# Kernel optimization log

Measured on AMD Instinct MI355X. Metric: run time of the kernel, lower is better.

The kernel has to match this reference:

```python
import jax, jax.numpy as jnp
import numpy as np
from jax import lax

B, T, D, H, K = 8, 1024, 1024, 16, 3
DK = D // H


def setup_inputs() -> dict:
    key = jax.random.key(0)
    ks = jax.random.split(key, 12)
    s = 0.02
    queries = jax.random.normal(ks[0], (B, T, D), dtype=jnp.float32)
    keys = jax.random.normal(ks[1], (B, T, D), dtype=jnp.float32)
    values = jax.random.normal(ks[2], (B, T, D), dtype=jnp.float32)
    # causal mask: True = masked (strict upper triangle)
    attn_mask = jnp.triu(jnp.ones((T, T), dtype=bool), k=1)
    # key padding mask: last 128 keys padded for every batch element
    src_key_padding_mask = jnp.broadcast_to(jnp.arange(T) >= T - 128, (B, T))
    conv_q_w = jax.random.normal(ks[3], (D, D, K), dtype=jnp.float32) * s  # (out, in, k)
    conv_q_b = jax.random.normal(ks[4], (D,), dtype=jnp.float32) * s
    conv_k_w = jax.random.normal(ks[5], (D, D, K), dtype=jnp.float32) * s
    conv_k_b = jax.random.normal(ks[6], (D,), dtype=jnp.float32) * s
    v_w = jax.random.normal(ks[7], (D, D), dtype=jnp.float32) * s   # torch Linear weight [out,in]
    v_b = jax.random.normal(ks[8], (D,), dtype=jnp.float32) * s
    out_w = jax.random.normal(ks[9], (D, D), dtype=jnp.float32) * s
    out_b = jax.random.normal(ks[10], (D,), dtype=jnp.float32) * s
    return {"queries": queries, "keys": keys, "values": values,
            "attn_mask": attn_mask, "src_key_padding_mask": src_key_padding_mask,
            "conv_q_w": conv_q_w, "conv_q_b": conv_q_b,
            "conv_k_w": conv_k_w, "conv_k_b": conv_k_b,
            "v_w": v_w, "v_b": v_b, "out_w": out_w, "out_b": out_b}


def _conv1d_same(x, w, b):
    # x: [B, T, D] -> conv over time with 'same' padding (pad_l=(K-1)//2, pad_r=K//2)
    pad_l, pad_r = (K - 1) // 2, K // 2
    xc = jnp.pad(x.transpose(0, 2, 1), ((0, 0), (0, 0), (pad_l, pad_r)))  # [B, D, T+K-1]
    y = lax.conv_general_dilated(xc, w, window_strides=(1,), padding='VALID',
                                 dimension_numbers=('NCH', 'OIH', 'NCH'))  # [B, D, T]
    return y.transpose(0, 2, 1) + b  # [B, T, D]


def _attention(queries, keys, values, attn_mask, key_padding_mask,
               conv_q_w, conv_q_b, conv_k_w, conv_k_b, v_w, v_b, out_w, out_b):
    q_out = _conv1d_same(queries, conv_q_w, conv_q_b)  # [B, Tq, D]
    k_out = _conv1d_same(keys, conv_k_w, conv_k_b)     # [B, Tk, D]
    v_out = values @ v_w.T + v_b                        # [B, Tk, D]

    Q = q_out.reshape(B, T, H, DK).transpose(0, 2, 1, 3)  # [B, H, Tq, dk]
    Kh = k_out.reshape(B, T, H, DK).transpose(0, 2, 1, 3)
    V = v_out.reshape(B, T, H, DK).transpose(0, 2, 1, 3)

    scores = jnp.einsum('bhqd,bhkd->bhqk', Q, Kh) / jnp.sqrt(jnp.float32(DK))
    neg = jnp.float32(-jnp.inf)
    scores = jnp.where(key_padding_mask[:, None, None, :], neg, scores)
    scores = jnp.where(attn_mask[None, None, :, :], neg, scores)
    attn_weights = jax.nn.softmax(scores, axis=-1)  # dropout is identity at eval
    attn_output = jnp.einsum('bhqk,bhkd->bhqd', attn_weights, V)
    attn_output = attn_output.transpose(0, 2, 1, 3).reshape(B, T, D)
    return attn_output @ out_w.T + out_b, attn_weights


def reference(queries, keys, values, attn_mask, src_key_padding_mask,
              conv_q_w, conv_q_b, conv_k_w, conv_k_b, v_w, v_b, out_w, out_b):
    return _attention(queries, keys, values, attn_mask, src_key_padding_mask,
                      conv_q_w, conv_q_b, conv_k_w, conv_k_b, v_w, v_b, out_w, out_b)
```

## Files before the change

### kernel.cpp

```cpp
#include <hip/hip_runtime.h>

typedef unsigned short u16;
typedef unsigned int   u32;
typedef __bf16 bf16x8 __attribute__((ext_vector_type(8)));
typedef float  f32x4  __attribute__((ext_vector_type(4)));
typedef const __attribute__((address_space(1))) u32* gas1_t;
typedef __attribute__((address_space(3))) u32*       las3_t;

#define DEV static __device__ __forceinline__
#define MFMA16(a, b, c) __builtin_amdgcn_mfma_f32_16x16x32_bf16((a), (b), (c), 0, 0, 0)

DEV u16 f2b(float f) {
  u32 u = __builtin_bit_cast(u32, f);
  return (u16)((u + 0x7fffu + ((u >> 16) & 1u)) >> 16);
}
DEV float b2f(u16 h) { return __builtin_bit_cast(float, (u32)h << 16); }

DEV void stage16(const void* g, void* l) {
  __builtin_amdgcn_global_load_lds((gas1_t)g, (las3_t)l, 16, 0, 0);
}

DEV int rfl(int x) { return __builtin_amdgcn_readfirstlane(x); }

extern "C" __global__ __launch_bounds__(256)
void k_prep(const float* __restrict__ s0, const float* __restrict__ s1,
            const float* __restrict__ s2, const float* __restrict__ s3,
            const float* __restrict__ s4, const float* __restrict__ wq,
            const float* __restrict__ wk, u16* __restrict__ dqkv,
            u16* __restrict__ dvw, u16* __restrict__ dow,
            u16* __restrict__ wtbase, u16* __restrict__ zbuf) {
  __shared__ float ls[3072];
  const int y = blockIdx.y, tid = threadIdx.x;
  if (y < 5) {
    const float* src = y == 0 ? s0 : y == 1 ? s1 : y == 2 ? s2 : y == 3 ? s3 : s4;
    u16* dst = y < 3 ? dqkv + (size_t)y * 8388608 : (y == 3 ? dvw : dow);
    const int n4 = y < 3 ? 2097152 : 262144;
    int i = blockIdx.x * 256 + tid;
    int st = gridDim.x * 256;
    for (; i < n4; i += st) {
      float4 v = ((const float4*)src)[i];
      ushort4 o;
      o.x = f2b(v.x); o.y = f2b(v.y); o.z = f2b(v.z); o.w = f2b(v.w);
      ((ushort4*)dst)[i] = o;
    }
  } else if (y < 7) {
    const int o = blockIdx.x, zz = y - 5;
    const float* src = (zz ? wk : wq) + (size_t)o * 3072;
#pragma unroll
    for (int s = 0; s < 3; ++s)
      ((float4*)ls)[s * 256 + tid] = ((const float4*)src)[s * 256 + tid];
    __syncthreads();
    u16* dst = wtbase + (size_t)zz * 3145728 + (size_t)o * 3072;
#pragma unroll
    for (int s = 0; s < 12; ++s) {
      int j = s * 256 + tid;
      int k = j >> 10, ii = j & 1023;
      dst[j] = f2b(ls[ii * 3 + k]);
    }
  } else {
    if (blockIdx.x == 0) zbuf[tid] = 0;
  }
}

template <int FUSED3, int OUTF32>
__global__ __launch_bounds__(256)
void k_gemm(const u16* __restrict__ Abase, const u16* __restrict__ Btbase,
            const float* __restrict__ b0, const float* __restrict__ b1,
            const float* __restrict__ b2, void* __restrict__ Cbase,
            u16* __restrict__ vT, const u16* __restrict__ zbuf) {
  __shared__ __align__(16) u16 smem[17408];
  const int z = FUSED3 ? blockIdx.z : 0;
  const bool conv = FUSED3 && (z < 2);
  const int K = conv ? 3072 : 1024;
  const u16* A = Abase + (size_t)z * 8388608;
  const u16* Bt = Btbase + (size_t)z * 3145728;
  const float* bias = z == 0 ? b0 : z == 1 ? b1 : b2;
  const int tid = threadIdx.x, lane = tid & 63, wave = tid >> 6;
  const int wm = wave >> 1, wn = wave & 1;
  const int l15 = lane & 15, gr = lane >> 4;
  const int r0 = blockIdx.y * 128, n0 = blockIdx.x * 128;
  const int srow = tid >> 3, scol = (tid & 7) * 8;
  u16* sA = smem;
  f32x4 acc[4][4] = {};

  if (conv) {
    u16* sB = smem + 8320;
    const int bb = r0 >> 10;
    const int tb = (r0 & 1023) - 1;
#pragma unroll 1
    for (int t = 0; t < 16; ++t) {
      const int c0 = t * 64;
#pragma unroll
      for (int s = 0; s < 5; ++s) {
        const int e = s * 256 + tid;
        if (e < 1040) {
          const int lr = e >> 3, ch = (e & 7) * 8;
          const int tt = tb + lr;
          const u16* g = ((u32)tt < 1024u)
              ? (A + (((size_t)((bb << 10) + tt)) << 10) + c0 + ch)
              : (zbuf + ch);
          stage16(g, (char*)smem + rfl((s * 256 + wave * 64) * 16));
        }
      }
#pragma unroll
      for (int s3 = 0; s3 < 3; ++s3) {
#pragma unroll
        for (int s = 0; s < 4; ++s) {
          const int row = s * 32 + srow;
          stage16(Bt + (size_t)(n0 + row) * 3072 + s3 * 1024 + c0 + scol,
                  (char*)smem + rfl(16640 + (s * 256 + wave * 64) * 16));
        }
        __syncthreads();
#pragma unroll
        for (int ks = 0; ks < 2; ++ks) {
          bf16x8 af[4], bfr[4];
          const int koff = ks * 32 + gr * 8;
#pragma unroll
          for (int f = 0; f < 4; ++f)
            af[f] = *(const bf16x8*)&sA[(wm * 64 + f * 16 + l15 + s3) * 64 + koff];
#pragma unroll
          for (int f = 0; f < 4; ++f)
            bfr[f] = *(const bf16x8*)&sB[(wn * 64 + f * 16 + l15) * 64 + koff];
#pragma unroll
          for (int i = 0; i < 4; ++i)
#pragma unroll
            for (int j = 0; j < 4; ++j)
              acc[i][j] = MFMA16(af[i], bfr[j], acc[i][j]);
        }
        __syncthreads();
      }
    }
  } else {
    u16* sB = smem + 8192;
    const int nt = K >> 6;
    for (int t = 0; t < nt; ++t) {
      const int k0 = t * 64;
#pragma unroll
      for (int s = 0; s < 4; ++s) {
        const int row = s * 32 + srow;
        stage16(A + (size_t)(r0 + row) * K + k0 + scol,
                (char*)smem + rfl((s * 256 + wave * 64) * 16));
        stage16(Bt + (size_t)(n0 + row) * K + k0 + scol,
                (char*)smem + rfl(16384 + (s * 256 + wave * 64) * 16));
      }
      __syncthreads();
#pragma unroll
      for (int ks = 0; ks < 2; ++ks) {
        bf16x8 af[4], bfr[4];
        const int koff = ks * 32 + gr * 8;
#pragma unroll
        for (int f = 0; f < 4; ++f)
          af[f] = *(const bf16x8*)&sA[(wm * 64 + f * 16 + l15) * 64 + koff];
#pragma unroll
        for (int f = 0; f < 4; ++f)
          bfr[f] = *(const bf16x8*)&sB[(wn * 64 + f * 16 + l15) * 64 + koff];
#pragma unroll
        for (int i = 0; i < 4; ++i)
#pragma unroll
          for (int j = 0; j < 4; ++j)
            acc[i][j] = MFMA16(af[i], bfr[j], acc[i][j]);
      }
      __syncthreads();
    }
  }

  if (FUSED3 && z == 2) {
    u16* tp = smem;
#pragma unroll
    for (int i = 0; i < 4; ++i)
#pragma unroll
      for (int j = 0; j < 4; ++j) {
        const int cl = wn * 64 + j * 16 + l15;
        const float bv = bias[n0 + cl];
        const int rl0 = wm * 64 + i * 16 + gr * 4;
        union { u16 h[4]; ushort4 v4; } tv;
#pragma unroll
        for (int r = 0; r < 4; ++r) tv.h[r] = f2b(acc[i][j][r] + bv);
        *(ushort4*)&tp[cl * 136 + rl0] = tv.v4;
      }
    __syncthreads();
    const int bb2 = r0 >> 10, tof = r0 & 1023;
    const int drb = tid >> 4, ch16 = (tid & 15) * 8;
#pragma unroll
    for (int g = 0; g < 8; ++g) {
      const int dr = g * 16 + drb;
      uint4 v4 = *(const uint4*)&tp[dr * 136 + ch16];
      *(uint4*)&vT[(((size_t)((bb2 << 10) + n0 + dr)) << 10) + tof + ch16] = v4;
    }
  } else {
    void* Cout = OUTF32 ? Cbase : (void*)((u16*)Cbase + (size_t)z * 8388608);
#pragma unroll
    for (int i = 0; i < 4; ++i)
#pragma unroll
      for (int j = 0; j < 4; ++j) {
        const int colg = n0 + wn * 64 + j * 16 + l15;
        const float bv = bias[colg];
#pragma unroll
        for (int r = 0; r < 4; ++r) {
          const int rowg = r0 + wm * 64 + i * 16 + gr * 4 + r;
          float v = acc[i][j][r] + bv;
          if (OUTF32) ((float*)Cout)[(size_t)rowg * 1024 + colg] = v;
          else        ((u16*)Cout)[(size_t)rowg * 1024 + colg] = f2b(v);
        }
      }
  }
}

__global__ __launch_bounds__(256)
void k_attn(const u16* __restrict__ Qg, const u16* __restrict__ Kg,
            const u16* __restrict__ Vtg, float* __restrict__ Wout,
            u16* __restrict__ Og) {
  __shared__ __align__(16) u16 sK[64 * 64];
  __shared__ __align__(16) u16 sV[64 * 64];
  __shared__ __align__(16) u16 sP[4][32 * 64];
  const int tid = threadIdx.x, lane = tid & 63, wave = tid >> 6;
  const int l15 = lane & 15, gr = lane >> 4;
  const int q0 = blockIdx.x * 128, h = blockIdx.y, b = blockIdx.z;
  const u16* Qh = Qg + ((size_t)b << 20) + h * 64;
  const u16* Kh = Kg + ((size_t)b << 20) + h * 64;
  const u16* Vh = Vtg + ((size_t)b << 20) + ((size_t)(h * 64) << 10);
  float* Wh = Wout + ((size_t)(b * 16 + h) << 20);
  const int qw0 = q0 + wave * 32;
  const int rmaxw = (qw0 + 31 < 895) ? (qw0 + 31) : 895;
  const int ktw = (rmaxw >> 6) + 1;
  const int rmaxg = (q0 + 127 < 895) ? (q0 + 127) : 895;
  const int ktmax = (rmaxg >> 6) + 1;

  bf16x8 qf[2][2];
#pragma unroll
  for (int i = 0; i < 2; ++i)
#pragma unroll
    for (int ks = 0; ks < 2; ++ks)
      qf[i][ks] = *(const bf16x8*)
          &Qh[(size_t)(qw0 + i * 16 + l15) * 1024 + ks * 32 + gr * 8];

  float lp[2][4] = {};

  for (int kt = 0; kt < ktmax; ++kt) {
#pragma unroll
    for (int s = 0; s < 2; ++s) {
      int e = s * 256 + tid;
      int row = e >> 3, col = (e & 7) * 8;
      stage16(Kh + (size_t)(kt * 64 + row) * 1024 + col,
              (char*)sK + rfl((s * 256 + wave * 64) * 16));
    }
    __syncthreads();
    if (kt < ktw) {
      f32x4 sc[2][4] = {};
#pragma unroll
      for (int ks = 0; ks < 2; ++ks) {
        bf16x8 bfr[4];
        const int koff = ks * 32 + gr * 8;
#pragma unroll
        for (int f = 0; f < 4; ++f)
          bfr[f] = *(const bf16x8*)&sK[(f * 16 + l15) * 64 + koff];
#pragma unroll
        for (int i = 0; i < 2; ++i)
#pragma unroll
          for (int f = 0; f < 4; ++f) sc[i][f] = MFMA16(qf[i][ks], bfr[f], sc[i][f]);
      }
#pragma unroll
      for (int i = 0; i < 2; ++i)
#pragma unroll
        for (int r = 0; r < 4; ++r) {
          const int rowg = qw0 + i * 16 + gr * 4 + r;
#pragma unroll
          for (int f = 0; f < 4; ++f) {
            const int colg = kt * 64 + f * 16 + l15;
            if (colg <= rowg) lp[i][r] += __expf(sc[i][f][r] * 0.125f);
          }
        }
    }
    __syncthreads();
  }

  float rl[2][4];
#pragma unroll
  for (int i = 0; i < 2; ++i)
#pragma unroll
    for (int r = 0; r < 4; ++r) {
      float ss = lp[i][r];
#pragma unroll
      for (int d = 1; d < 16; d <<= 1) ss += __shfl_xor(ss, d, 16);
      rl[i][r] = 1.f / ss;
    }

  for (int r = 0; r < 32; ++r) {
    float* wrow = Wh + (size_t)(qw0 + r) * 1024;
    for (int c = ktw * 64 + lane * 4; c < 1024; c += 256)
      *(float4*)&wrow[c] = make_float4(0.f, 0.f, 0.f, 0.f);
  }

  f32x4 oa[2][4] = {};
  for (int kt = 0; kt < ktmax; ++kt) {
#pragma unroll
    for (int s = 0; s < 2; ++s) {
      int e = s * 256 + tid;
      int row = e >> 3, col = (e & 7) * 8;
      stage16(Kh + (size_t)(kt * 64 + row) * 1024 + col,
              (char*)sK + rfl((s * 256 + wave * 64) * 16));
      stage16(Vh + (size_t)row * 1024 + kt * 64 + col,
              (char*)sV + rfl((s * 256 + wave * 64) * 16));
    }
    __syncthreads();
    if (kt < ktw) {
      f32x4 sc[2][4] = {};
#pragma unroll
      for (int ks = 0; ks < 2; ++ks) {
        bf16x8 bfr[4];
        const int koff = ks * 32 + gr * 8;
#pragma unroll
        for (int f = 0; f < 4; ++f)
          bfr[f] = *(const bf16x8*)&sK[(f * 16 + l15) * 64 + koff];
#pragma unroll
        for (int i = 0; i < 2; ++i)
#pragma unroll
          for (int f = 0; f < 4; ++f) sc[i][f] = MFMA16(qf[i][ks], bfr[f], sc[i][f]);
      }
#pragma unroll
      for (int i = 0; i < 2; ++i)
#pragma unroll
        for (int r = 0; r < 4; ++r) {
          const int rowl = i * 16 + gr * 4 + r;
          const int rowg = qw0 + rowl;
#pragma unroll
          for (int f = 0; f < 4; ++f) {
            const int colt = f * 16 + l15;
            const int colg = kt * 64 + colt;
            float p = (colg <= rowg)
                          ? __expf(sc[i][f][r] * 0.125f) * rl[i][r] : 0.f;
            sP[wave][rowl * 64 + colt] = f2b(p);
          }
        }
      asm volatile("s_waitcnt lgkmcnt(0)" ::: "memory");
#pragma unroll
      for (int ks = 0; ks < 2; ++ks) {
        bf16x8 paf[2], vf[4];
        const int koff = ks * 32 + gr * 8;
        paf[0] = *(const bf16x8*)&sP[wave][l15 * 64 + koff];
        paf[1] = *(const bf16x8*)&sP[wave][(16 + l15) * 64 + koff];
#pragma unroll
        for (int f = 0; f < 4; ++f)
          vf[f] = *(const bf16x8*)&sV[(f * 16 + l15) * 64 + koff];
#pragma unroll
        for (int i = 0; i < 2; ++i)
#pragma unroll
          for (int f = 0; f < 4; ++f) oa[i][f] = MFMA16(paf[i], vf[f], oa[i][f]);
      }
#pragma unroll
      for (int rr = 0; rr < 8; ++rr) {
        const int rowl = rr * 4 + gr;
        const int c4 = l15 * 4;
        union { u16 h[4]; uint2 v2; } t;
        t.v2 = *(const uint2*)&sP[wave][rowl * 64 + c4];
        float4 o;
        o.x = b2f(t.h[0]); o.y = b2f(t.h[1]); o.z = b2f(t.h[2]); o.w = b2f(t.h[3]);
        *(float4*)&Wh[(size_t)(qw0 + rowl) * 1024 + kt * 64 + c4] = o;
      }
    }
    __syncthreads();
  }
#pragma unroll
  for (int i = 0; i < 2; ++i)
#pragma unroll
    for (int f = 0; f < 4; ++f)
#pragma unroll
      for (int r = 0; r < 4; ++r) {
        const int rowg = qw0 + i * 16 + gr * 4 + r;
        const int dd = f * 16 + l15;
        Og[((size_t)b * 1024 + rowg) * 1024 + h * 64 + dd] = f2b(oa[i][f][r]);
      }
}

extern "C" void kernel_launch(void* const* d_in, const int* in_sizes, int n_in,
                              void* d_out, int out_size, void* d_ws, size_t ws_size,
                              hipStream_t stream) {
  const float* queries  = (const float*)d_in[0];
  const float* keys     = (const float*)d_in[1];
  const float* values   = (const float*)d_in[2];
  const float* conv_q_w = (const float*)d_in[5];
  const float* conv_q_b = (const float*)d_in[6];
  const float* conv_k_w = (const float*)d_in[7];
  const float* conv_k_b = (const float*)d_in[8];
  const float* v_w      = (const float*)d_in[9];
  const float* v_b      = (const float*)d_in[10];
  const float* out_w    = (const float*)d_in[11];
  const float* out_b    = (const float*)d_in[12];

  float* out0 = (float*)d_out;
  float* outW = out0 + (size_t)8 * 1024 * 1024;

  char* W = (char*)d_ws;
  u16* qkv_bf = (u16*)(W + (size_t)0);
  u16* wt     = (u16*)(W + (size_t)50331648);
  u16* ow_t   = (u16*)(W + (size_t)65011712);
  u16* q_out  = (u16*)(W + (size_t)67108864);
  u16* zbuf   = (u16*)(W + (size_t)117440512);
  u16* vw_t   = wt + (size_t)2 * 3145728;
  u16* k_out  = q_out + (size_t)8388608;
  u16* v_outT = q_out + (size_t)2 * 8388608;
  u16* a_out  = qkv_bf + 8388608;

  dim3 blk(256);
  k_prep<<<dim3(1024, 8), blk, 0, stream>>>(queries, keys, values, v_w, out_w,
                                            conv_q_w, conv_k_w, qkv_bf, vw_t,
                                            ow_t, wt, zbuf);

  k_gemm<1, 0><<<dim3(8, 64, 3), blk, 0, stream>>>(
      qkv_bf, wt, conv_q_b, conv_k_b, v_b, (void*)q_out, v_outT, zbuf);
  k_attn<<<dim3(8, 16, 8), blk, 0, stream>>>(q_out, k_out, v_outT, outW, a_out);
  k_gemm<0, 1><<<dim3(8, 64, 1), blk, 0, stream>>>(
      a_out, ow_t, out_b, out_b, out_b, (void*)out0, v_outT, zbuf);
}
```

Baseline: 436.5 us.

## Use 32x32 MFMA with XOR-swizzled LDS in conv GEMM path

The conv branch of the fused QKV GEMM now uses 32x32x16 bf16 MFMA tiles (2x2 per wave) instead of 16x16x32 tiles (4x4). The A and B staging into LDS applies an XOR swizzle on 16-byte chunk index by row, so the 32-row fragment reads avoid bank conflicts. The conv path gets its own epilogue that writes bf16 output with bias directly from the 32x32 accumulator layout and returns early. The risk is that these scattered per-element 2-byte stores are uncoalesced compared with the shared epilogue.

```diff
diff --git a/kernel.cpp b/kernel.cpp
--- a/kernel.cpp
+++ b/kernel.cpp
@@ -4,11 +4,13 @@
 typedef unsigned int   u32;
 typedef __bf16 bf16x8 __attribute__((ext_vector_type(8)));
 typedef float  f32x4  __attribute__((ext_vector_type(4)));
+typedef float  f32x16 __attribute__((ext_vector_type(16)));
 typedef const __attribute__((address_space(1))) u32* gas1_t;
 typedef __attribute__((address_space(3))) u32*       las3_t;
 
 #define DEV static __device__ __forceinline__
 #define MFMA16(a, b, c) __builtin_amdgcn_mfma_f32_16x16x32_bf16((a), (b), (c), 0, 0, 0)
+#define MFMA32(a, b, c) __builtin_amdgcn_mfma_f32_32x32x16_bf16((a), (b), (c), 0, 0, 0)
 
 DEV u16 f2b(float f) {
   u32 u = __builtin_bit_cast(u32, f);
@@ -81,12 +83,13 @@
   const int r0 = blockIdx.y * 128, n0 = blockIdx.x * 128;
   const int srow = tid >> 3, scol = (tid & 7) * 8;
   u16* sA = smem;
-  f32x4 acc[4][4] = {};
 
   if (conv) {
     u16* sB = smem + 8320;
+    const int l31 = lane & 31, hi = lane >> 5;
     const int bb = r0 >> 10;
     const int tb = (r0 & 1023) - 1;
+    f32x16 acc32[2][2] = {};
 #pragma unroll 1
     for (int t = 0; t < 16; ++t) {
       const int c0 = t * 64;
@@ -94,11 +97,12 @@
       for (int s = 0; s < 5; ++s) {
         const int e = s * 256 + tid;
         if (e < 1040) {
-          const int lr = e >> 3, ch = (e & 7) * 8;
+          const int lr = e >> 3;
+          const int jg = (e & 7) ^ (lr & 7);
           const int tt = tb + lr;
           const u16* g = ((u32)tt < 1024u)
-              ? (A + (((size_t)((bb << 10) + tt)) << 10) + c0 + ch)
-              : (zbuf + ch);
+              ? (A + (((size_t)((bb << 10) + tt)) << 10) + c0 + jg * 8)
+              : (zbuf + jg * 8);
           stage16(g, (char*)smem + rfl((s * 256 + wave * 64) * 16));
         }
       }
@@ -107,61 +111,82 @@
 #pragma unroll
         for (int s = 0; s < 4; ++s) {
           const int row = s * 32 + srow;
-          stage16(Bt + (size_t)(n0 + row) * 3072 + s3 * 1024 + c0 + scol,
+          const int jg = (tid & 7) ^ (row & 7);
+          stage16(Bt + (size_t)(n0 + row) * 3072 + s3 * 1024 + c0 + jg * 8,
                   (char*)smem + rfl(16640 + (s * 256 + wave * 64) * 16));
         }
         __syncthreads();
 #pragma unroll
-        for (int ks = 0; ks < 2; ++ks) {
-          bf16x8 af[4], bfr[4];
-          const int koff = ks * 32 + gr * 8;
-#pragma unroll
-          for (int f = 0; f < 4; ++f)
-            af[f] = *(const bf16x8*)&sA[(wm * 64 + f * 16 + l15 + s3) * 64 + koff];
-#pragma unroll
-          for (int f = 0; f < 4; ++f)
-            bfr[f] = *(const bf16x8*)&sB[(wn * 64 + f * 16 + l15) * 64 + koff];
-#pragma unroll
-          for (int i = 0; i < 4; ++i)
-#pragma unroll
-            for (int j = 0; j < 4; ++j)
-              acc[i][j] = MFMA16(af[i], bfr[j], acc[i][j]);
+        for (int kk = 0; kk < 4; ++kk) {
+          const int gq = kk * 2 + hi;
+          bf16x8 af[2], bfr[2];
+#pragma unroll
+          for (int mi = 0; mi < 2; ++mi) {
+            const int ra = wm * 64 + mi * 32 + l31 + s3;
+            af[mi] = *(const bf16x8*)&sA[ra * 64 + ((gq ^ (ra & 7)) * 8)];
+          }
+#pragma unroll
+          for (int nj = 0; nj < 2; ++nj) {
+            const int rb = wn * 64 + nj * 32 + l31;
+            bfr[nj] = *(const bf16x8*)&sB[rb * 64 + ((gq ^ (rb & 7)) * 8)];
+          }
+#pragma unroll
+          for (int mi = 0; mi < 2; ++mi)
+#pragma unroll
+            for (int nj = 0; nj < 2; ++nj)
+              acc32[mi][nj] = MFMA32(af[mi], bfr[nj], acc32[mi][nj]);
         }
         __syncthreads();
       }
     }
-  } else {
-    u16* sB = smem + 8192;
-    const int nt = K >> 6;
-    for (int t = 0; t < nt; ++t) {
-      const int k0 = t * 64;
-#pragma unroll
-      for (int s = 0; s < 4; ++s) {
-        const int row = s * 32 + srow;
-        stage16(A + (size_t)(r0 + row) * K + k0 + scol,
-                (char*)smem + rfl((s * 256 + wave * 64) * 16));
-        stage16(Bt + (size_t)(n0 + row) * K + k0 + scol,
-                (char*)smem + rfl(16384 + (s * 256 + wave * 64) * 16));
-      }
-      __syncthreads();
-#pragma unroll
-      for (int ks = 0; ks < 2; ++ks) {
-        bf16x8 af[4], bfr[4];
-        const int koff = ks * 32 + gr * 8;
-#pragma unroll
-        for (int f = 0; f < 4; ++f)
-          af[f] = *(const bf16x8*)&sA[(wm * 64 + f * 16 + l15) * 64 + koff];
-#pragma unroll
-        for (int f = 0; f < 4; ++f)
-          bfr[f] = *(const bf16x8*)&sB[(wn * 64 + f * 16 + l15) * 64 + koff];
-#pragma unroll
-        for (int i = 0; i < 4; ++i)
-#pragma unroll
-          for (int j = 0; j < 4; ++j)
-            acc[i][j] = MFMA16(af[i], bfr[j], acc[i][j]);
-      }
-      __syncthreads();
-    }
+    u16* Cout = (u16*)Cbase + (size_t)z * 8388608;
+#pragma unroll
+    for (int mi = 0; mi < 2; ++mi)
+#pragma unroll
+      for (int nj = 0; nj < 2; ++nj) {
+        const int colg = n0 + wn * 64 + nj * 32 + l31;
+        const float bv = bias[colg];
+#pragma unroll
+        for (int reg = 0; reg < 16; ++reg) {
+          const int rowg =
+              r0 + wm * 64 + mi * 32 + (reg & 3) + 8 * (reg >> 2) + 4 * hi;
+          Cout[(size_t)rowg * 1024 + colg] = f2b(acc32[mi][nj][reg] + bv);
+        }
+      }
+    return;
+  }
+
+  f32x4 acc[4][4] = {};
+  u16* sB = smem + 8192;
+  const int nt = K >> 6;
+  for (int t = 0; t < nt; ++t) {
+    const int k0 = t * 64;
+#pragma unroll
+    for (int s = 0; s < 4; ++s) {
+      const int row = s * 32 + srow;
+      stage16(A + (size_t)(r0 + row) * K + k0 + scol,
+              (char*)smem + rfl((s * 256 + wave * 64) * 16));
+      stage16(Bt + (size_t)(n0 + row) * K + k0 + scol,
+              (char*)smem + rfl(16384 + (s * 256 + wave * 64) * 16));
+    }
+    __syncthreads();
+#pragma unroll
+    for (int ks = 0; ks < 2; ++ks) {
+      bf16x8 af[4], bfr[4];
+      const int koff = ks * 32 + gr * 8;
+#pragma unroll
+      for (int f = 0; f < 4; ++f)
+        af[f] = *(const bf16x8*)&sA[(wm * 64 + f * 16 + l15) * 64 + koff];
+#pragma unroll
+      for (int f = 0; f < 4; ++f)
+        bfr[f] = *(const bf16x8*)&sB[(wn * 64 + f * 16 + l15) * 64 + koff];
+#pragma unroll
+      for (int i = 0; i < 4; ++i)
+#pragma unroll
+        for (int j = 0; j < 4; ++j)
+          acc[i][j] = MFMA16(af[i], bfr[j], acc[i][j]);
+    }
+    __syncthreads();
   }
 
   if (FUSED3 && z == 2) {
```

New measurement: 414.1 us. 1.05x faster.
